# Kernel optimization log

Hardware: AMD Instinct MI355X
Metric: run time of the kernel (lower is better)

## Reference

```python
import jax, jax.numpy as jnp
import numpy as np

T, B, D, R, H = 16, 1024, 1024, 8, 16
DH = D // H


def setup_inputs() -> dict:
    key = jax.random.key(0)
    ks = jax.random.split(key, 10)
    s = 1.0 / np.sqrt(D)
    return {
        "table_embs": jax.random.normal(ks[0], (T, B, D), jnp.float32),
        "rel_embs": jax.random.normal(ks[1], (T, R, D), jnp.float32),
        "rel_idx": jax.random.randint(ks[2], (T, R), 0, T),
        "Wq": jax.random.normal(ks[3], (D, D), jnp.float32) * s,
        "bq": jnp.zeros((D,), jnp.float32),
        "Wk": jax.random.normal(ks[4], (D, D), jnp.float32) * s,
        "bk": jnp.zeros((D,), jnp.float32),
        "Wv": jax.random.normal(ks[5], (D, D), jnp.float32) * s,
        "bv": jnp.zeros((D,), jnp.float32),
        "Wo": jax.random.normal(ks[6], (D, D), jnp.float32) * s,
        "bo": jnp.zeros((D,), jnp.float32),
        "w_rel": jax.random.normal(ks[7], (D,), jnp.float32) * s,
        "b_rel": jnp.zeros((1,), jnp.float32),
    }


def reference(table_embs, rel_embs, rel_idx, Wq, bq, Wk, bk, Wv, bv, Wo, bo, w_rel, b_rel):
    # relationship weights: sigmoid(Linear(rel_emb)) -> scalar per (table, relation)
    rel_w = jax.nn.sigmoid(rel_embs @ w_rel + b_rel[0])          # [T, R]
    # gather related tables' embeddings and apply relationship weight
    others = table_embs[rel_idx]                                  # [T, R, B, D]
    weighted = others * rel_w[:, :, None, None]                   # [T, R, B, D]
    kv_src = jnp.transpose(weighted, (0, 2, 1, 3))                # [T, B, R, D]
    # MultiheadAttention, q_len=1, kv_len=R (PyTorch convention: x @ W.T + b)
    q = (table_embs @ Wq.T + bq).reshape(T, B, H, DH)             # [T, B, H, DH]
    k = (kv_src @ Wk.T + bk).reshape(T, B, R, H, DH)              # [T, B, R, H, DH]
    v = (kv_src @ Wv.T + bv).reshape(T, B, R, H, DH)
    scores = jnp.einsum("tbhd,tbrhd->tbhr", q, k) / np.sqrt(DH)   # [T, B, H, R]
    attn = jax.nn.softmax(scores, axis=-1)
    ctx = jnp.einsum("tbhr,tbrhd->tbhd", attn, v).reshape(T, B, D)
    return ctx @ Wo.T + bo                                        # [T, B, D]
```

## Files before the change

kernel.cpp:

```cpp
#include <hip/hip_runtime.h>


typedef unsigned short u16;
typedef __attribute__((ext_vector_type(8))) short short8;
typedef __attribute__((ext_vector_type(4))) float f32x4;

__device__ __forceinline__ float bf2f(u16 u) {
  unsigned int x = ((unsigned int)u) << 16;
  return __uint_as_float(x);
}
__device__ __forceinline__ u16 f2bf(float f) {
  unsigned int x = __float_as_uint(f);
  unsigned int r = (x + 0x7fffu + ((x >> 16) & 1u)) >> 16;
  return (u16)r;
}

__device__ __forceinline__ void gld_lds16(const void* g, void* l) {
  __builtin_amdgcn_global_load_lds(
      (const __attribute__((address_space(1))) unsigned int*)(unsigned long long)g,
      (__attribute__((address_space(3))) unsigned int*)(unsigned int)(unsigned long long)l,
      16, 0, 0);
}


__global__ void relw_kernel(const float* __restrict__ rel_embs,
                            const float* __restrict__ w_rel,
                            const float* __restrict__ b_rel,
                            float* __restrict__ rel_w) {
  const int tr = blockIdx.x;
  const float* row = rel_embs + (size_t)tr * 1024;
  const int lane = threadIdx.x;
  float s = 0.f;
  for (int i = lane; i < 1024; i += 64) s += row[i] * w_rel[i];
  for (int off = 32; off > 0; off >>= 1) s += __shfl_down(s, off, 64);
  if (lane == 0) rel_w[tr] = 1.f / (1.f + __expf(-(s + b_rel[0])));
}

__global__ void cvt_f32_bf16(const float* __restrict__ in, u16* __restrict__ out, int n4) {
  int i = blockIdx.x * blockDim.x + threadIdx.x;
  if (i >= n4) return;
  float4 v = ((const float4*)in)[i];
  ushort4 o;
  o.x = f2bf(v.x); o.y = f2bf(v.y); o.z = f2bf(v.z); o.w = f2bf(v.w);
  ((ushort4*)out)[i] = o;
}

__global__ void cvt_w4(const float* __restrict__ Wq, const float* __restrict__ Wk,
                       const float* __restrict__ Wv, const float* __restrict__ Wo,
                       u16* __restrict__ Wcat, u16* __restrict__ Wob) {
  const int i = blockIdx.x * 256 + threadIdx.x;
  const int w = i >> 18;
  const int j = i & 0x3ffff;
  const float* src = (w == 0) ? Wq : (w == 1) ? Wk : (w == 2) ? Wv : Wo;
  u16* dst = (w == 3) ? Wob : (Wcat + ((size_t)w << 20));
  float4 v = ((const float4*)src)[j];
  ushort4 o;
  o.x = f2bf(v.x); o.y = f2bf(v.y); o.z = f2bf(v.z); o.w = f2bf(v.w);
  ((ushort4*)dst)[j] = o;
}


__device__ __forceinline__ void gemm_mainloop(const u16* __restrict__ A,
                                              const u16* __restrict__ B,
                                              u16* As, u16* Bs,
                                              int m0, int n0, int K,
                                              f32x4 (&acc)[4][4]) {
  const int tid  = threadIdx.x;
  const int wave = tid >> 6;
  const int lane = tid & 63;

  const int srow   = wave * 32 + (lane >> 2);
  const int gchunk = (lane & 3) ^ ((lane >> 3) & 3);
  const u16* pa0 = A + (size_t)(m0 + srow) * K + gchunk * 8;
  const u16* pa1 = pa0 + (size_t)16 * K;
  const u16* pb0 = B + (size_t)(n0 + srow) * K + gchunk * 8;
  const u16* pb1 = pb0 + (size_t)16 * K;
  u16* la0 = As + wave * 1024;
  u16* la1 = la0 + 512;
  u16* lb0 = Bs + wave * 1024;
  u16* lb1 = lb0 + 512;

  const int fr  = lane & 15;
  const int fq  = lane >> 4;
  const int swz = (fr >> 1) & 3;
  const int mb = (wave >> 1) * 64;
  const int nb = (wave & 1) * 64;

  for (int k0 = 0; k0 < K; k0 += 32) {
    gld_lds16(pa0, la0); gld_lds16(pa1, la1);
    gld_lds16(pb0, lb0); gld_lds16(pb1, lb1);
    pa0 += 32; pa1 += 32; pb0 += 32; pb1 += 32;
    __syncthreads();
    short8 af[4], bg[4];
#pragma unroll
    for (int i = 0; i < 4; ++i) {
      af[i] = *(const short8*)(As + (mb + i * 16 + fr) * 32 + (fq ^ swz) * 8);
      bg[i] = *(const short8*)(Bs + (nb + i * 16 + fr) * 32 + (fq ^ swz) * 8);
    }
#pragma unroll
    for (int i = 0; i < 4; ++i)
#pragma unroll
      for (int j = 0; j < 4; ++j)
        acc[i][j] = __builtin_amdgcn_mfma_f32_16x16x32_bf16(af[i], bg[j], acc[i][j], 0, 0, 0);
    __syncthreads();
  }
}

__global__ __launch_bounds__(256)
void gemm_qkv(const u16* __restrict__ A, const u16* __restrict__ B,
              const float* __restrict__ bq,
              u16* __restrict__ Qt, u16* __restrict__ Kt, u16* __restrict__ Vt) {
  __shared__ __align__(16) u16 smem[128 * 136];
  u16* As = smem;
  u16* Bs = smem + 4096;
  const int m0 = blockIdx.y * 128;
  const int n0 = blockIdx.x * 128;
  f32x4 acc[4][4];
#pragma unroll
  for (int i = 0; i < 4; ++i)
#pragma unroll
    for (int j = 0; j < 4; ++j) acc[i][j] = (f32x4){0.f, 0.f, 0.f, 0.f};

  gemm_mainloop(A, B, As, Bs, m0, n0, 1024, acc);

  const int lane = threadIdx.x & 63;
  const int wave = threadIdx.x >> 6;
  const int mb = (wave >> 1) * 64, nb = (wave & 1) * 64;
  const int colw = lane & 15, roww = (lane >> 4) * 4;
  const int sel = n0 >> 10;

#pragma unroll
  for (int i = 0; i < 4; ++i) {
#pragma unroll
    for (int j = 0; j < 4; ++j) {
      const int dl = nb + j * 16 + colw;
      const float badd = (sel == 0) ? bq[n0 + dl] : 0.f;
#pragma unroll
      for (int r = 0; r < 4; ++r) {
        const int bl = mb + i * 16 + roww + r;
        smem[dl * 136 + bl] = f2bf(acc[i][j][r] + badd);
      }
    }
  }
  __syncthreads();
  {
    const int row  = threadIdx.x >> 1;
    const int half = threadIdx.x & 1;
    const int t = m0 >> 10, b0 = m0 & 1023;
    u16* basep = (sel == 0) ? Qt : (sel == 1) ? Kt : Vt;
    u16* dp = basep + ((size_t)t << 20) + (size_t)((n0 - (sel << 10)) + row) * 1024
            + b0 + half * 64;
    const u16* sp = smem + row * 136 + half * 64;
#pragma unroll
    for (int c = 0; c < 8; ++c)
      ((uint4*)dp)[c] = ((const uint4*)sp)[c];
  }
}

__global__ __launch_bounds__(256)
void gemm_out(const u16* __restrict__ A, const u16* __restrict__ B,
              const float* __restrict__ bo, float* __restrict__ out) {
  __shared__ __align__(16) u16 As[4096];
  __shared__ __align__(16) u16 Bs[4096];
  const int m0 = blockIdx.y * 128;
  const int n0 = blockIdx.x * 128;
  f32x4 acc[4][4];
#pragma unroll
  for (int i = 0; i < 4; ++i)
#pragma unroll
    for (int j = 0; j < 4; ++j) acc[i][j] = (f32x4){0.f, 0.f, 0.f, 0.f};

  gemm_mainloop(A, B, As, Bs, m0, n0, 1024, acc);

  const int lane = threadIdx.x & 63;
  const int wave = threadIdx.x >> 6;
  const int mb = (wave >> 1) * 64, nb = (wave & 1) * 64;
  const int colw = lane & 15, roww = (lane >> 4) * 4;
#pragma unroll
  for (int i = 0; i < 4; ++i) {
#pragma unroll
    for (int j = 0; j < 4; ++j) {
      const int gn = n0 + nb + j * 16 + colw;
#pragma unroll
      for (int r = 0; r < 4; ++r) {
        const int gm = m0 + mb + i * 16 + roww + r;
        out[(size_t)gm * 1024 + gn] = acc[i][j][r] + bo[gn];
      }
    }
  }
}

__global__ __launch_bounds__(256)
void attn5(const u16* __restrict__ Qt, const u16* __restrict__ Kt,
           const u16* __restrict__ Vt,
           const float* __restrict__ relw, const int* __restrict__ rel_idx,
           const float* __restrict__ bk, const float* __restrict__ bv,
           u16* __restrict__ ctx) {
  const int tid = threadIdx.x;
  const int h = blockIdx.y, t = blockIdx.z;
  const int b0 = blockIdx.x * 256;
  const int b = b0 + tid;
  const int hd = h * 64;

  __shared__ u16  st[256 * 34];
  __shared__ float bks[64], bvs[64], rws[8];
  __shared__ int   rids[8];

  if (tid < 64) { bks[tid] = bk[hd + tid]; bvs[tid] = bv[hd + tid]; }
  else if (tid < 72) { rws[tid - 64] = relw[t * 8 + (tid - 64)];
                       rids[tid - 64] = rel_idx[t * 8 + (tid - 64)]; }
  __syncthreads();

  const unsigned qoff = ((unsigned)t << 20) + ((unsigned)hd << 10) + (unsigned)b;
  unsigned koff[8];
#pragma unroll
  for (int r = 0; r < 8; ++r)
    koff[r] = ((unsigned)rids[r] << 20) + ((unsigned)hd << 10) + (unsigned)b;

  float acc[8];
#pragma unroll
  for (int r = 0; r < 8; ++r) acc[r] = 0.f;
  float qbk = 0.f;
#pragma unroll 4
  for (int d = 0; d < 64; ++d) {
    const float q = bf2f(Qt[qoff + d * 1024]);
    qbk += q * bks[d];
#pragma unroll
    for (int r = 0; r < 8; ++r)
      acc[r] += q * bf2f(Kt[koff[r] + d * 1024]);
  }

  float w[8];
  {
    float s[8], mx = -1e30f;
#pragma unroll
    for (int r = 0; r < 8; ++r) {
      s[r] = (rws[r] * acc[r] + qbk) * 0.125f;
      mx = fmaxf(mx, s[r]);
    }
    float sum = 0.f;
#pragma unroll
    for (int r = 0; r < 8; ++r) { s[r] = __expf(s[r] - mx); sum += s[r]; }
    const float inv = 1.f / sum;
#pragma unroll
    for (int r = 0; r < 8; ++r) w[r] = s[r] * inv * rws[r];
  }

  for (int half = 0; half < 2; ++half) {
#pragma unroll
    for (int dp = 0; dp < 32; dp += 2) {
      const int d = half * 32 + dp;
      float o0 = bvs[d];
      float o1 = bvs[d + 1];
#pragma unroll
      for (int r = 0; r < 8; ++r) {
        o0 += w[r] * bf2f(Vt[koff[r] + d * 1024]);
        o1 += w[r] * bf2f(Vt[koff[r] + (d + 1) * 1024]);
      }
      const unsigned p = (unsigned)f2bf(o0) | ((unsigned)f2bf(o1) << 16);
      *(unsigned*)(st + tid * 34 + dp) = p;
    }
    __syncthreads();
    {
      const int sub = tid & 7;
      const int rbase = tid >> 3;
#pragma unroll
      for (int p = 0; p < 8; ++p) {
        const int row = p * 32 + rbase;
        const uint2 v = *(const uint2*)(st + row * 34 + sub * 4);
        *(uint2*)(ctx + ((size_t)(t * 1024 + b0 + row)) * 1024
                  + hd + half * 32 + sub * 4) = v;
      }
    }
    __syncthreads();
  }
}


extern "C" void kernel_launch(void* const* d_in, const int* in_sizes, int n_in,
                              void* d_out, int out_size, void* d_ws, size_t ws_size,
                              hipStream_t stream) {
  const float* table = (const float*)d_in[0];
  const float* rele  = (const float*)d_in[1];
  const int*   ridx  = (const int*)d_in[2];
  const float* Wq    = (const float*)d_in[3];
  const float* bq    = (const float*)d_in[4];
  const float* Wk    = (const float*)d_in[5];
  const float* bk    = (const float*)d_in[6];
  const float* Wv    = (const float*)d_in[7];
  const float* bv    = (const float*)d_in[8];
  const float* Wo    = (const float*)d_in[9];
  const float* bo    = (const float*)d_in[10];
  const float* wr    = (const float*)d_in[11];
  const float* br    = (const float*)d_in[12];
  float* out = (float*)d_out;

  char* ws = (char*)d_ws;
  const size_t MB = 1024 * 1024;
  u16*  Xbf  = (u16*)(ws);
  u16*  Kt   = (u16*)(ws + 32  * MB);
  u16*  Vt   = (u16*)(ws + 64  * MB);
  u16*  Qt   = (u16*)(ws + 96  * MB);
  u16*  Wcat = (u16*)(ws + 128 * MB);
  u16*  Wob  = (u16*)(ws + 134 * MB);
  float* relw = (float*)(ws + 136 * MB);
  u16*  ctxb = Xbf;

  relw_kernel<<<128, 64, 0, stream>>>(rele, wr, br, relw);
  cvt_f32_bf16<<<16384, 256, 0, stream>>>(table, Xbf, 4194304);
  cvt_w4<<<4096, 256, 0, stream>>>(Wq, Wk, Wv, Wo, Wcat, Wob);

  gemm_qkv<<<dim3(24, 128), 256, 0, stream>>>(Xbf, Wcat, bq, Qt, Kt, Vt);
  attn5<<<dim3(4, 16, 16), 256, 0, stream>>>(Qt, Kt, Vt, relw, ridx, bk, bv, ctxb);
  gemm_out<<<dim3(8, 128), 256, 0, stream>>>(ctxb, Wob, bo, out);
}
```

Baseline: 420.7 us.

## Rewrite GEMM mainloop with 256x256 tiles, double-buffered LDS, and phased MFMA scheduling

Both the QKV and output GEMMs move from 128x128 tiles with a single LDS buffer and 256 threads to 256x256 tiles run by 512 threads. The new mainloop uses BK=64, double-buffers A/B in 128KB of LDS, and overlaps global-to-LDS loads for the next k-tile with MFMA work on the current one. It also adds explicit barriers, s_setprio and sched_barrier hints. The QKV epilogue transposes through LDS in two passes with packed bf16 stores. This cuts per-iteration syncs and raises arithmetic intensity, but the large LDS footprint limits occupancy and the grid shrinks to 768 and 256 blocks, which may underfill the GPU.

```diff
diff --git a/kernel.cpp b/kernel.cpp
--- a/kernel.cpp
+++ b/kernel.cpp
@@ -60,132 +60,187 @@
 }
 
 
-__device__ __forceinline__ void gemm_mainloop(const u16* __restrict__ A,
-                                              const u16* __restrict__ B,
-                                              u16* As, u16* Bs,
-                                              int m0, int n0, int K,
-                                              f32x4 (&acc)[4][4]) {
+__device__ __forceinline__ void mainloop256(const u16* __restrict__ A,
+                                            const u16* __restrict__ B,
+                                            u16* lds, int m0, int n0,
+                                            f32x4 (&acc)[8][4]) {
   const int tid  = threadIdx.x;
-  const int wave = tid >> 6;
   const int lane = tid & 63;
-
-  const int srow   = wave * 32 + (lane >> 2);
-  const int gchunk = (lane & 3) ^ ((lane >> 3) & 3);
-  const u16* pa0 = A + (size_t)(m0 + srow) * K + gchunk * 8;
-  const u16* pa1 = pa0 + (size_t)16 * K;
-  const u16* pb0 = B + (size_t)(n0 + srow) * K + gchunk * 8;
-  const u16* pb1 = pb0 + (size_t)16 * K;
-  u16* la0 = As + wave * 1024;
-  u16* la1 = la0 + 512;
-  u16* lb0 = Bs + wave * 1024;
-  u16* lb1 = lb0 + 512;
-
-  const int fr  = lane & 15;
-  const int fq  = lane >> 4;
-  const int swz = (fr >> 1) & 3;
-  const int mb = (wave >> 1) * 64;
-  const int nb = (wave & 1) * 64;
-
-  for (int k0 = 0; k0 < K; k0 += 32) {
-    gld_lds16(pa0, la0); gld_lds16(pa1, la1);
-    gld_lds16(pb0, lb0); gld_lds16(pb1, lb1);
-    pa0 += 32; pa1 += 32; pb0 += 32; pb1 += 32;
-    __syncthreads();
-    short8 af[4], bg[4];
-#pragma unroll
-    for (int i = 0; i < 4; ++i) {
-      af[i] = *(const short8*)(As + (mb + i * 16 + fr) * 32 + (fq ^ swz) * 8);
-      bg[i] = *(const short8*)(Bs + (nb + i * 16 + fr) * 32 + (fq ^ swz) * 8);
-    }
-#pragma unroll
-    for (int i = 0; i < 4; ++i)
-#pragma unroll
-      for (int j = 0; j < 4; ++j)
-        acc[i][j] = __builtin_amdgcn_mfma_f32_16x16x32_bf16(af[i], bg[j], acc[i][j], 0, 0, 0);
-    __syncthreads();
-  }
-}
-
-__global__ __launch_bounds__(256)
-void gemm_qkv(const u16* __restrict__ A, const u16* __restrict__ B,
+  const int w    = tid >> 6;
+  const int wm   = w >> 2, wn = w & 3;
+  const int fr   = lane & 15, fq = lane >> 4;
+  const int swz  = fr & 7;
+
+  const unsigned A0 = 0, B0 = 16384, A1 = 32768, B1 = 49152;
+
+  const int srow = tid >> 3;
+  const int lc   = (tid & 7) ^ (srow & 7);
+  const u16* a0p = A + (size_t)(m0 + srow) * 1024 + lc * 8;
+  const u16* b0p = B + (size_t)(n0 + srow) * 1024 + lc * 8;
+  const unsigned d0 = (unsigned)((tid & ~63) * 8);
+
+  const u16 *ap0[2], *ap1[2], *bp0[2], *bp1[2];
+#pragma unroll
+  for (int ks = 0; ks < 2; ++ks) {
+    const unsigned ck = (unsigned)((((ks << 2) + fq) ^ swz) << 3);
+    ap0[ks] = lds + A0 + (wm * 128 + fr) * 64 + ck;
+    ap1[ks] = lds + A1 + (wm * 128 + fr) * 64 + ck;
+    bp0[ks] = lds + B0 + (wn * 64 + fr) * 64 + ck;
+    bp1[ks] = lds + B1 + (wn * 64 + fr) * 64 + ck;
+  }
+
+#define STAGE4(g, AO, BO)                                                      \
+  do {                                                                         \
+    gld_lds16(a0p + (2*(g))   * 65536, lds + (AO) + d0 + (2*(g))   * 4096);    \
+    gld_lds16(a0p + (2*(g)+1) * 65536, lds + (AO) + d0 + (2*(g)+1) * 4096);    \
+    gld_lds16(b0p + (2*(g))   * 65536, lds + (BO) + d0 + (2*(g))   * 4096);    \
+    gld_lds16(b0p + (2*(g)+1) * 65536, lds + (BO) + d0 + (2*(g)+1) * 4096);    \
+  } while (0)
+
+#define PHASE_Q(q, ap, STMT)                                                   \
+  do {                                                                         \
+    short8 a0k0 = *(const short8*)((ap)[0] + (2*(q))   * 1024);                \
+    short8 a1k0 = *(const short8*)((ap)[0] + (2*(q)+1) * 1024);                \
+    short8 a0k1 = *(const short8*)((ap)[1] + (2*(q))   * 1024);                \
+    short8 a1k1 = *(const short8*)((ap)[1] + (2*(q)+1) * 1024);                \
+    STMT;                                                                      \
+    __builtin_amdgcn_s_barrier();                                              \
+    asm volatile("s_waitcnt lgkmcnt(0)" ::: "memory");                         \
+    __builtin_amdgcn_sched_barrier(0);                                         \
+    __builtin_amdgcn_s_setprio(1);                                             \
+    _Pragma("unroll")                                                          \
+    for (int j = 0; j < 4; ++j) {                                              \
+      acc[2*(q)][j]   = __builtin_amdgcn_mfma_f32_16x16x32_bf16(a0k0, bgv[j][0], acc[2*(q)][j],   0, 0, 0); \
+      acc[2*(q)+1][j] = __builtin_amdgcn_mfma_f32_16x16x32_bf16(a1k0, bgv[j][0], acc[2*(q)+1][j], 0, 0, 0); \
+    }                                                                          \
+    _Pragma("unroll")                                                          \
+    for (int j = 0; j < 4; ++j) {                                              \
+      acc[2*(q)][j]   = __builtin_amdgcn_mfma_f32_16x16x32_bf16(a0k1, bgv[j][1], acc[2*(q)][j],   0, 0, 0); \
+      acc[2*(q)+1][j] = __builtin_amdgcn_mfma_f32_16x16x32_bf16(a1k1, bgv[j][1], acc[2*(q)+1][j], 0, 0, 0); \
+    }                                                                          \
+    __builtin_amdgcn_s_setprio(0);                                             \
+  } while (0)
+
+#define KTILE(ap, bp, AO_N, BO_N, SG)                                          \
+  do {                                                                         \
+    short8 bgv[4][2];                                                          \
+    _Pragma("unroll")                                                          \
+    for (int j = 0; j < 4; ++j) {                                              \
+      bgv[j][0] = *(const short8*)((bp)[0] + j * 1024);                        \
+      bgv[j][1] = *(const short8*)((bp)[1] + j * 1024);                        \
+    }                                                                          \
+    PHASE_Q(0, ap, { if (SG) STAGE4(0, AO_N, BO_N); });                        \
+    __builtin_amdgcn_s_barrier();                                              \
+    PHASE_Q(1, ap, { if (SG) { STAGE4(1, AO_N, BO_N); a0p += 64; b0p += 64; } }); \
+    __builtin_amdgcn_s_barrier();                                              \
+    PHASE_Q(2, ap, {});                                                        \
+    __builtin_amdgcn_s_barrier();                                              \
+    PHASE_Q(3, ap, {});                                                        \
+    if (SG) asm volatile("s_waitcnt vmcnt(0)" ::: "memory");                   \
+    __builtin_amdgcn_s_barrier();                                              \
+  } while (0)
+
+#pragma unroll
+  for (int r = 0; r < 4; ++r) {
+    gld_lds16(a0p + r * 65536, lds + A0 + d0 + r * 4096);
+    gld_lds16(b0p + r * 65536, lds + B0 + d0 + r * 4096);
+  }
+  a0p += 64; b0p += 64;
+  asm volatile("s_waitcnt vmcnt(0)" ::: "memory");
+  __builtin_amdgcn_s_barrier();
+
+  for (int it = 0; it < 8; ++it) {
+    KTILE(ap0, bp0, A1, B1, true);
+    KTILE(ap1, bp1, A0, B0, (it < 7));
+  }
+#undef STAGE4
+#undef PHASE_Q
+#undef KTILE
+}
+
+__global__ __launch_bounds__(512, 2)
+void gemm_qkv(const u16* __restrict__ A, const u16* __restrict__ Bw,
               const float* __restrict__ bq,
               u16* __restrict__ Qt, u16* __restrict__ Kt, u16* __restrict__ Vt) {
-  __shared__ __align__(16) u16 smem[128 * 136];
-  u16* As = smem;
-  u16* Bs = smem + 4096;
-  const int m0 = blockIdx.y * 128;
-  const int n0 = blockIdx.x * 128;
-  f32x4 acc[4][4];
-#pragma unroll
-  for (int i = 0; i < 4; ++i)
+  __shared__ __align__(16) u16 lds[65536];
+  const int n0 = blockIdx.x * 256;
+  const int m0 = blockIdx.y * 256;
+  f32x4 acc[8][4];
+#pragma unroll
+  for (int i = 0; i < 8; ++i)
 #pragma unroll
     for (int j = 0; j < 4; ++j) acc[i][j] = (f32x4){0.f, 0.f, 0.f, 0.f};
 
-  gemm_mainloop(A, B, As, Bs, m0, n0, 1024, acc);
+  mainloop256(A, Bw, lds, m0, n0, acc);
+
+  const int tid  = threadIdx.x;
+  const int lane = tid & 63;
+  const int w    = tid >> 6;
+  const int wm   = w >> 2, wn = w & 3;
+  const int colw = lane & 15, roww = (lane >> 4) * 4;
+  const int t = m0 >> 10, b0 = m0 & 1023;
+  const int sel = n0 >> 10, dbase = n0 & 1023;
+  u16* outp = (sel == 0) ? Qt : (sel == 1) ? Kt : Vt;
+
+  for (int pass = 0; pass < 2; ++pass) {
+    if (wm == pass) {
+#pragma unroll
+      for (int j = 0; j < 4; ++j) {
+        const int dl = wn * 64 + j * 16 + colw;
+        const float badd = (sel == 0) ? bq[dbase + dl] : 0.f;
+#pragma unroll
+        for (int i = 0; i < 8; ++i) {
+          const int bl = i * 16 + roww;
+          const unsigned p0 = (unsigned)f2bf(acc[i][j][0] + badd)
+                            | ((unsigned)f2bf(acc[i][j][1] + badd) << 16);
+          const unsigned p1 = (unsigned)f2bf(acc[i][j][2] + badd)
+                            | ((unsigned)f2bf(acc[i][j][3] + badd) << 16);
+          *(unsigned*)(lds + dl * 136 + bl)     = p0;
+          *(unsigned*)(lds + dl * 136 + bl + 2) = p1;
+        }
+      }
+    }
+    __syncthreads();
+#pragma unroll
+    for (int rr = 0; rr < 8; ++rr) {
+      const int slot = rr * 512 + tid;
+      const int row = slot >> 4, c16 = slot & 15;
+      const uint4 v = *(const uint4*)(lds + row * 136 + c16 * 8);
+      *(uint4*)(outp + ((size_t)t << 20) + (size_t)(dbase + row) * 1024
+                + b0 + pass * 128 + c16 * 8) = v;
+    }
+    __syncthreads();
+  }
+}
+
+__global__ __launch_bounds__(512, 2)
+void gemm_out(const u16* __restrict__ A, const u16* __restrict__ Bw,
+              const float* __restrict__ bo, float* __restrict__ out) {
+  __shared__ __align__(16) u16 lds[65536];
+  const int n0 = blockIdx.x * 256;
+  const int m0 = blockIdx.y * 256;
+  f32x4 acc[8][4];
+#pragma unroll
+  for (int i = 0; i < 8; ++i)
+#pragma unroll
+    for (int j = 0; j < 4; ++j) acc[i][j] = (f32x4){0.f, 0.f, 0.f, 0.f};
+
+  mainloop256(A, Bw, lds, m0, n0, acc);
 
   const int lane = threadIdx.x & 63;
-  const int wave = threadIdx.x >> 6;
-  const int mb = (wave >> 1) * 64, nb = (wave & 1) * 64;
+  const int w    = threadIdx.x >> 6;
+  const int wm   = w >> 2, wn = w & 3;
   const int colw = lane & 15, roww = (lane >> 4) * 4;
-  const int sel = n0 >> 10;
-
-#pragma unroll
-  for (int i = 0; i < 4; ++i) {
-#pragma unroll
-    for (int j = 0; j < 4; ++j) {
-      const int dl = nb + j * 16 + colw;
-      const float badd = (sel == 0) ? bq[n0 + dl] : 0.f;
-#pragma unroll
-      for (int r = 0; r < 4; ++r) {
-        const int bl = mb + i * 16 + roww + r;
-        smem[dl * 136 + bl] = f2bf(acc[i][j][r] + badd);
-      }
-    }
-  }
-  __syncthreads();
-  {
-    const int row  = threadIdx.x >> 1;
-    const int half = threadIdx.x & 1;
-    const int t = m0 >> 10, b0 = m0 & 1023;
-    u16* basep = (sel == 0) ? Qt : (sel == 1) ? Kt : Vt;
-    u16* dp = basep + ((size_t)t << 20) + (size_t)((n0 - (sel << 10)) + row) * 1024
-            + b0 + half * 64;
-    const u16* sp = smem + row * 136 + half * 64;
-#pragma unroll
-    for (int c = 0; c < 8; ++c)
-      ((uint4*)dp)[c] = ((const uint4*)sp)[c];
-  }
-}
-
-__global__ __launch_bounds__(256)
-void gemm_out(const u16* __restrict__ A, const u16* __restrict__ B,
-              const float* __restrict__ bo, float* __restrict__ out) {
-  __shared__ __align__(16) u16 As[4096];
-  __shared__ __align__(16) u16 Bs[4096];
-  const int m0 = blockIdx.y * 128;
-  const int n0 = blockIdx.x * 128;
-  f32x4 acc[4][4];
-#pragma unroll
-  for (int i = 0; i < 4; ++i)
-#pragma unroll
-    for (int j = 0; j < 4; ++j) acc[i][j] = (f32x4){0.f, 0.f, 0.f, 0.f};
-
-  gemm_mainloop(A, B, As, Bs, m0, n0, 1024, acc);
-
-  const int lane = threadIdx.x & 63;
-  const int wave = threadIdx.x >> 6;
-  const int mb = (wave >> 1) * 64, nb = (wave & 1) * 64;
-  const int colw = lane & 15, roww = (lane >> 4) * 4;
-#pragma unroll
-  for (int i = 0; i < 4; ++i) {
-#pragma unroll
-    for (int j = 0; j < 4; ++j) {
-      const int gn = n0 + nb + j * 16 + colw;
-#pragma unroll
-      for (int r = 0; r < 4; ++r) {
-        const int gm = m0 + mb + i * 16 + roww + r;
-        out[(size_t)gm * 1024 + gn] = acc[i][j][r] + bo[gn];
-      }
+#pragma unroll
+  for (int j = 0; j < 4; ++j) {
+    const int gn = n0 + wn * 64 + j * 16 + colw;
+    const float bov = bo[gn];
+#pragma unroll
+    for (int i = 0; i < 8; ++i) {
+      const int gm = m0 + wm * 128 + i * 16 + roww;
+#pragma unroll
+      for (int r = 0; r < 4; ++r)
+        out[(size_t)(gm + r) * 1024 + gn] = acc[i][j][r] + bov;
     }
   }
 }
@@ -310,7 +365,7 @@
   cvt_f32_bf16<<<16384, 256, 0, stream>>>(table, Xbf, 4194304);
   cvt_w4<<<4096, 256, 0, stream>>>(Wq, Wk, Wv, Wo, Wcat, Wob);
 
-  gemm_qkv<<<dim3(24, 128), 256, 0, stream>>>(Xbf, Wcat, bq, Qt, Kt, Vt);
+  gemm_qkv<<<dim3(12, 64), 512, 0, stream>>>(Xbf, Wcat, bq, Qt, Kt, Vt);
   attn5<<<dim3(4, 16, 16), 256, 0, stream>>>(Qt, Kt, Vt, relw, ridx, bk, bv, ctxb);
-  gemm_out<<<dim3(8, 128), 256, 0, stream>>>(ctxb, Wob, bo, out);
-}
+  gemm_out<<<dim3(4, 64), 512, 0, stream>>>(ctxb, Wob, bo, out);
+}
```

Measured after the change: 371.5 us. -11.7%, faster.
